# Optimization experiments

Hardware: AMD Instinct MI355X
Metric: run time of the kernel (lower is better)

## Reference

```python
import jax, jax.numpy as jnp
import numpy as np

NEG_SLOPE = 0.2


def _gat_layer(x, W, a_src, a_dst, src, dst, ew, num_nodes):
    # Dense projection: [N, Din] @ [Din, Dout] -> [N, Dout]
    h = x @ W
    s = h @ a_src  # per-node source score, [N]
    d = h @ a_dst  # per-node destination score, [N]
    score = jax.nn.leaky_relu(s[src] + d[dst], NEG_SLOPE)  # [E]
    # segment softmax over incoming edges of each destination node
    m = jax.ops.segment_max(score, dst, num_segments=num_nodes)
    ex = jnp.exp(score - m[dst])
    denom = jax.ops.segment_sum(ex, dst, num_segments=num_nodes)
    alpha = ex / jnp.maximum(denom[dst], jnp.asarray(1e-16, ex.dtype))
    alpha = alpha * ew  # edge-weighted attention
    # gather h_j, scale by alpha, scatter-add into destinations
    return jax.ops.segment_sum(h[src] * alpha[:, None], dst, num_segments=num_nodes)


def setup_inputs() -> dict:
    key = jax.random.key(0)
    ks = jax.random.split(key, 9)
    N, E, F_IN, HID, NC = 100000, 1600000, 256, 64, 40
    x = jax.random.normal(ks[0], (N, F_IN), dtype=jnp.float32)
    edge_index = jax.random.randint(ks[1], (2, E), 0, N, dtype=jnp.int32)
    edge_weight = jax.random.uniform(ks[2], (E,), dtype=jnp.float32)
    W1 = jax.random.normal(ks[3], (F_IN, HID), dtype=jnp.float32) / np.sqrt(F_IN)
    a1_src = jax.random.normal(ks[4], (HID,), dtype=jnp.float32) / np.sqrt(HID)
    a1_dst = jax.random.normal(ks[5], (HID,), dtype=jnp.float32) / np.sqrt(HID)
    W2 = jax.random.normal(ks[6], (HID, NC), dtype=jnp.float32) / np.sqrt(HID)
    a2_src = jax.random.normal(ks[7], (NC,), dtype=jnp.float32) / np.sqrt(NC)
    a2_dst = jax.random.normal(ks[8], (NC,), dtype=jnp.float32) / np.sqrt(NC)
    return {"x": x, "edge_index": edge_index, "edge_weight": edge_weight,
            "W1": W1, "a1_src": a1_src, "a1_dst": a1_dst,
            "W2": W2, "a2_src": a2_src, "a2_dst": a2_dst}


def reference(x, edge_index, edge_weight, W1, a1_src, a1_dst, W2, a2_src, a2_dst):
    N = x.shape[0]
    # add_self_loops=True in both convs: append (i, i) edges with weight 1
    loops = jnp.arange(N, dtype=edge_index.dtype)
    src = jnp.concatenate([edge_index[0], loops])
    dst = jnp.concatenate([edge_index[1], loops])
    ew = jnp.concatenate([edge_weight, jnp.ones((N,), edge_weight.dtype)])
    h = jax.nn.relu(_gat_layer(x, W1, a1_src, a1_dst, src, dst, ew, N))
    # dropout inactive in eval mode
    out = _gat_layer(h, W2, a2_src, a2_dst, src, dst, ew, N)
    return out
```

## Files before the change

kernel.cpp:

```cpp
#include <hip/hip_runtime.h>
#include <hip/hip_bf16.h>
#include <math.h>

#define NEG_SLOPE 0.2f

typedef __attribute__((ext_vector_type(4))) float f32x4;
typedef __attribute__((ext_vector_type(8))) short bf16x8;
typedef __attribute__((ext_vector_type(4))) short bf16x4;

__device__ __forceinline__ float leaky(float x) { return x > 0.f ? x : NEG_SLOPE * x; }

__device__ __forceinline__ unsigned short bf_hi(float x) {
  return (unsigned short)(__float_as_uint(x) >> 16);
}

__device__ __forceinline__ unsigned short bf_rne(float x) {
  unsigned u = __float_as_uint(x);
  return (unsigned short)((u + 0x7FFFu + ((u >> 16) & 1u)) >> 16);
}


#define BIN_CHUNK 2048
#define BCAP 8192

__global__ void k_curinit(int* __restrict__ cursor, int NB) {
  int i = blockIdx.x * blockDim.x + threadIdx.x;
  if (i < NB) cursor[i] = i * BCAP;
}

__global__ __launch_bounds__(256)
void k_bin(const int* __restrict__ ei, const float* __restrict__ ew, int E, int N,
           int* __restrict__ cursor, int2* __restrict__ staged, int NB) {
  __shared__ int lhist[512];
  __shared__ int lbase[512];
  int tid = threadIdx.x;
  int start = blockIdx.x * BIN_CHUNK;
  int NT = E + N;
  int srcv[8], dstv[8]; float wv[8];
#pragma unroll
  for (int j = 0; j < 8; j++) {
    int e = start + j * 256 + tid;
    int s = 0, d = -1; float w = 0.f;
    if (e < NT) {
      if (e < E) { s = ei[e]; d = ei[E + e]; w = ew[e]; }
      else       { s = d = e - E; w = 1.f; }
    }
    srcv[j] = s; dstv[j] = d; wv[j] = w;
  }
  for (int b = tid; b < NB; b += 256) lhist[b] = 0;
  __syncthreads();
#pragma unroll
  for (int j = 0; j < 8; j++)
    if (dstv[j] >= 0) atomicAdd(&lhist[dstv[j] >> 8], 1);
  __syncthreads();
  for (int b = tid; b < NB; b += 256) {
    int n = lhist[b];
    lbase[b] = (n > 0) ? atomicAdd(&cursor[b], n) : 0;
    lhist[b] = 0;
  }
  __syncthreads();
#pragma unroll
  for (int j = 0; j < 8; j++) {
    if (dstv[j] >= 0) {
      int bkt = dstv[j] >> 8;
      int off = atomicAdd(&lhist[bkt], 1);
      staged[lbase[bkt] + off] =
          make_int2(srcv[j] | ((dstv[j] & 255) << 24), __float_as_int(wv[j]));
    }
  }
}

__global__ __launch_bounds__(512)
void k_bscan(const int* __restrict__ cursor, int NB, int NT, int N,
             int* __restrict__ bbase, int* __restrict__ rp) {
  __shared__ int sm[512];
  int tid = threadIdx.x;
  int v = (tid < NB) ? cursor[tid] - tid * BCAP : 0;
  sm[tid] = v;
  __syncthreads();
  for (int off = 1; off < 512; off <<= 1) {
    int x = sm[tid];
    int a = (tid >= off) ? sm[tid - off] : 0;
    __syncthreads();
    sm[tid] = x + a;
    __syncthreads();
  }
  if (tid < NB) bbase[tid] = sm[tid] - v;
  if (tid == 0) { bbase[NB] = sm[NB - 1]; rp[N] = NT; }
}

__global__ __launch_bounds__(512)
void k_finalize(const int2* __restrict__ staged, const int* __restrict__ bbase,
                int N, int* __restrict__ rp, int2* __restrict__ csr) {
  __shared__ int cnt[256];
  __shared__ int sm[256];
  int b = blockIdx.x, tid = threadIdx.x;
  int sbase = b * BCAP;
  int cbase = bbase[b];
  int size = bbase[b + 1] - cbase;
  if (tid < 256) cnt[tid] = 0;
  __syncthreads();
  for (int i = tid; i < size; i += 512) {
    int2 v = staged[sbase + i];
    atomicAdd(&cnt[((unsigned)v.x) >> 24], 1);
  }
  __syncthreads();
  int s = 0;
  if (tid < 256) { s = cnt[tid]; sm[tid] = s; }
  __syncthreads();
  for (int off = 1; off < 256; off <<= 1) {
    int x = 0;
    if (tid < 256) { x = sm[tid]; if (tid >= off) x += sm[tid - off]; }
    __syncthreads();
    if (tid < 256) sm[tid] = x;
    __syncthreads();
  }
  if (tid < 256) {
    int excl = sm[tid] - s;
    int node = (b << 8) + tid;
    if (node < N) rp[node] = cbase + excl;
    cnt[tid] = excl;
  }
  __syncthreads();
  for (int i = tid; i < size; i += 512) {
    int2 v = staged[sbase + i];
    int dlow = ((unsigned)v.x) >> 24;
    int pos = cbase + atomicAdd(&cnt[dlow], 1);
    csr[pos] = make_int2(v.x & 0x00FFFFFF, v.y);
  }
}

__global__ __launch_bounds__(256)
void k_wprep(const float* __restrict__ W, int K, int Mout,
             unsigned short* __restrict__ whi, unsigned short* __restrict__ wlo) {
  int idx = blockIdx.x * 256 + threadIdx.x;
  if (idx >= K * 64) return;
  int k = idx >> 6, n = idx & 63;
  float v = (n < Mout) ? W[(size_t)k * Mout + n] : 0.f;
  unsigned short h = bf_hi(v);
  float hf = __uint_as_float((unsigned)h << 16);
  unsigned short l = bf_hi(v - hf);
  int kc = k >> 5, kk = k & 31, quad = kk >> 3, j = kk & 7;
  int ct = n >> 4, nn = n & 15;
  int off = (((kc * 4 + ct) * 64) + quad * 16 + nn) * 8 + j;
  whi[off] = h; wlo[off] = l;
}

__global__ __launch_bounds__(256)
void k_gemm_mfma(const float* __restrict__ X, int K,
                 const unsigned short* __restrict__ WHI, const unsigned short* __restrict__ WLO,
                 const float* __restrict__ ASRC, const float* __restrict__ ADST, int Mout,
                 float* __restrict__ Hf, unsigned short* __restrict__ Hb, int ldH,
                 float* __restrict__ S, float* __restrict__ D, int N) {
  __shared__ __align__(16) unsigned short xhi[2048], xlo[2048];
  __shared__ __align__(16) unsigned short whs[2048], wls[2048];
  int tid = threadIdx.x;
  int lane = tid & 63, w = tid >> 6;
  int rowBase = blockIdx.x * 64;

  f32x4 acc[4];
#pragma unroll
  for (int c = 0; c < 4; c++) acc[c] = (f32x4){0.f, 0.f, 0.f, 0.f};

  int q0 = tid, q1 = tid + 256;
  int row0 = q0 >> 3, k40 = (q0 & 7) << 2;
  int row1 = q1 >> 3, k41 = (q1 & 7) << 2;
  int xo0 = (((row0 >> 4) * 64) + (k40 >> 3) * 16 + (row0 & 15)) * 8 + (k40 & 7);
  int xo1 = (((row1 >> 4) * 64) + (k41 >> 3) * 16 + (row1 & 15)) * 8 + (k41 & 7);
  int grow0 = rowBase + row0, grow1 = rowBase + row1;

  int nch = K >> 5;
  f32x4 xr0, xr1; bf16x8 wh, wl;

  xr0 = (f32x4){0.f, 0.f, 0.f, 0.f}; xr1 = xr0;
  if (grow0 < N) xr0 = *(const f32x4*)&X[(size_t)grow0 * K + k40];
  if (grow1 < N) xr1 = *(const f32x4*)&X[(size_t)grow1 * K + k41];
  wh = *(const bf16x8*)(WHI + tid * 8);
  wl = *(const bf16x8*)(WLO + tid * 8);

  for (int kc = 0; kc < nch; kc++) {
    bf16x4 h4, l4;
#pragma unroll
    for (int i = 0; i < 4; i++) {
      unsigned short h = bf_hi(xr0[i]);
      float hf = __uint_as_float((unsigned)h << 16);
      h4[i] = (short)h; l4[i] = (short)bf_hi(xr0[i] - hf);
    }
    *(bf16x4*)(xhi + xo0) = h4; *(bf16x4*)(xlo + xo0) = l4;
#pragma unroll
    for (int i = 0; i < 4; i++) {
      unsigned short h = bf_hi(xr1[i]);
      float hf = __uint_as_float((unsigned)h << 16);
      h4[i] = (short)h; l4[i] = (short)bf_hi(xr1[i] - hf);
    }
    *(bf16x4*)(xhi + xo1) = h4; *(bf16x4*)(xlo + xo1) = l4;
    *(bf16x8*)(whs + tid * 8) = wh;
    *(bf16x8*)(wls + tid * 8) = wl;
    __syncthreads();

    if (kc + 1 < nch) {
      int kb = (kc + 1) << 5;
      xr0 = (f32x4){0.f, 0.f, 0.f, 0.f}; xr1 = xr0;
      if (grow0 < N) xr0 = *(const f32x4*)&X[(size_t)grow0 * K + kb + k40];
      if (grow1 < N) xr1 = *(const f32x4*)&X[(size_t)grow1 * K + kb + k41];
      wh = *(const bf16x8*)(WHI + (size_t)(kc + 1) * 2048 + tid * 8);
      wl = *(const bf16x8*)(WLO + (size_t)(kc + 1) * 2048 + tid * 8);
    }

    bf16x8 ah = *(const bf16x8*)(xhi + (w * 64 + lane) * 8);
    bf16x8 al = *(const bf16x8*)(xlo + (w * 64 + lane) * 8);
#pragma unroll
    for (int c = 0; c < 4; c++) {
      bf16x8 bh = *(const bf16x8*)(whs + (c * 64 + lane) * 8);
      bf16x8 bl = *(const bf16x8*)(wls + (c * 64 + lane) * 8);
      acc[c] = __builtin_amdgcn_mfma_f32_16x16x32_bf16(ah, bh, acc[c], 0, 0, 0);
      acc[c] = __builtin_amdgcn_mfma_f32_16x16x32_bf16(ah, bl, acc[c], 0, 0, 0);
      acc[c] = __builtin_amdgcn_mfma_f32_16x16x32_bf16(al, bh, acc[c], 0, 0, 0);
    }
    __syncthreads();
  }

  int nn = lane & 15, quad = lane >> 4;
  float as_[4], ad_[4];
#pragma unroll
  for (int c = 0; c < 4; c++) {
    int col = c * 16 + nn;
    as_[c] = (col < Mout) ? ASRC[col] : 0.f;
    ad_[c] = (col < Mout) ? ADST[col] : 0.f;
  }
#pragma unroll
  for (int r = 0; r < 4; r++) {
    int grow = rowBase + w * 16 + quad * 4 + r;
    float ps = 0.f, pd = 0.f;
#pragma unroll
    for (int c = 0; c < 4; c++) {
      float v = acc[c][r];
      int col = c * 16 + nn;
      if (grow < N && col < Mout) {
        if (Hb) Hb[(size_t)grow * ldH + col] = bf_rne(v);
        else    Hf[(size_t)grow * ldH + col] = v;
      }
      ps += v * as_[c]; pd += v * ad_[c];
    }
#pragma unroll
    for (int off = 1; off < 16; off <<= 1) {
      ps += __shfl_xor(ps, off);
      pd += __shfl_xor(pd, off);
    }
    if (nn == 0 && grow < N) { S[grow] = ps; D[grow] = pd; }
  }
}

template <bool BF16>
__global__ __launch_bounds__(256)
void k_agg_fused(const int* __restrict__ rp, const int2* __restrict__ csr,
                 const float* __restrict__ S, const float* __restrict__ D,
                 const void* __restrict__ HinV, int ldh,
                 float* __restrict__ Out, int F4, int ldo, int do_relu, int N) {
  int gw = (blockIdx.x * blockDim.x + threadIdx.x) >> 6;
  int lane = threadIdx.x & 63;
  int sub = lane >> 4, fl = lane & 15;
  int node = gw * 4 + sub;
  bool active = node < N;
  bool fless = fl < F4;
  int b = 0, e = 1; float dd = 0.f;
  if (active) { b = rp[node]; e = rp[node + 1]; dd = D[node]; }
  float den = 0.f;
  f32x4 acc0 = (f32x4){0.f, 0.f, 0.f, 0.f};
  f32x4 acc1 = (f32x4){0.f, 0.f, 0.f, 0.f};

  int need = e - b;
  need = max(need, __shfl_xor(need, 16));
  need = max(need, __shfl_xor(need, 32));
  int iters = (need + 3) >> 2;
  int last = e - 1;

  int t = b;
  for (int it = 0; it < iters; it++, t += 4) {
    int  idx[4]; float wgt[4], sv[4], ex[4]; f32x4 hv[4];
#pragma unroll
    for (int j = 0; j < 4; j++) {
      int tj = t + j < e ? t + j : last;
      int2 p = csr[tj];
      idx[j] = p.x;
      wgt[j] = (t + j < e) ? __int_as_float(p.y) : 0.f;
    }
#pragma unroll
    for (int j = 0; j < 4; j++) sv[j] = S[idx[j]];
#pragma unroll
    for (int j = 0; j < 4; j++) {
      hv[j] = (f32x4){0.f, 0.f, 0.f, 0.f};
      if (fless && (t + j < e)) {
        if (BF16) {
          const unsigned short* Hb = (const unsigned short*)HinV;
          ushort4 uv = *(const ushort4*)(Hb + (size_t)idx[j] * ldh + (fl << 2));
          hv[j][0] = __uint_as_float((unsigned)uv.x << 16);
          hv[j][1] = __uint_as_float((unsigned)uv.y << 16);
          hv[j][2] = __uint_as_float((unsigned)uv.z << 16);
          hv[j][3] = __uint_as_float((unsigned)uv.w << 16);
        } else {
          const float* Hf = (const float*)HinV;
          hv[j] = *(const f32x4*)&Hf[(size_t)idx[j] * ldh + (fl << 2)];
        }
      }
    }
#pragma unroll
    for (int j = 0; j < 4; j++)
      ex[j] = (t + j < e) ? __expf(leaky(sv[j] + dd)) : 0.f;
    den += (ex[0] + ex[1]) + (ex[2] + ex[3]);
    acc0 += hv[0] * (ex[0] * wgt[0]) + hv[1] * (ex[1] * wgt[1]);
    acc1 += hv[2] * (ex[2] * wgt[2]) + hv[3] * (ex[3] * wgt[3]);
  }

  if (active && fless) {
    float inv = 1.0f / fmaxf(den, 1e-16f);
    f32x4 o = (acc0 + acc1) * inv;
    if (do_relu) {
#pragma unroll
      for (int j = 0; j < 4; j++) o[j] = fmaxf(o[j], 0.f);
    }
    *(f32x4*)&Out[(size_t)node * ldo + (fl << 2)] = o;
  }
}

extern "C" void kernel_launch(void* const* d_in, const int* in_sizes, int n_in,
                              void* d_out, int out_size, void* d_ws, size_t ws_size,
                              hipStream_t stream) {
  const float* x   = (const float*)d_in[0];
  const int*   ei  = (const int*)d_in[1];
  const float* ew  = (const float*)d_in[2];
  const float* W1  = (const float*)d_in[3];
  const float* a1s = (const float*)d_in[4];
  const float* a1d = (const float*)d_in[5];
  const float* W2  = (const float*)d_in[6];
  const float* a2s = (const float*)d_in[7];
  const float* a2d = (const float*)d_in[8];

  const int HID = in_sizes[4];
  const int NC  = in_sizes[7];
  const int FIN = in_sizes[3] / HID;
  const int N   = in_sizes[0] / FIN;
  const int E   = in_sizes[2];
  const int NT  = E + N;
  const int NB  = (N + 255) >> 8;
  float* out = (float*)d_out;

  char* wsb = (char*)d_ws;
  size_t off = 0;
  auto alloc = [&](size_t bytes) -> char* {
    char* p = wsb + off;
    off += (bytes + 255) & ~(size_t)255;
    return p;
  };
  unsigned short* h1b = (unsigned short*)alloc((size_t)N * 64 * 2);
  float* h2     = (float*)alloc((size_t)N * 64 * 4);
  float* g2     = (float*)alloc((size_t)N * 48 * 4);
  float* S      = (float*)alloc((size_t)N * 4);
  float* D      = (float*)alloc((size_t)N * 4);
  int*   rp     = (int*)alloc((size_t)(N + 1) * 4);
  int*   bbase  = (int*)alloc((size_t)(NB + 1) * 4);
  int*   cursor = (int*)alloc((size_t)NB * 4);
  int2*  csr    = (int2*)alloc((size_t)NT * 8);
  int2*  staged = (int2*)alloc((size_t)NB * BCAP * 8);
  unsigned short* whi1 = (unsigned short*)alloc((size_t)FIN * 64 * 2);
  unsigned short* wlo1 = (unsigned short*)alloc((size_t)FIN * 64 * 2);
  unsigned short* whi2 = (unsigned short*)alloc((size_t)HID * 64 * 2);
  unsigned short* wlo2 = (unsigned short*)alloc((size_t)HID * 64 * 2);
  (void)ws_size; (void)n_in; (void)out_size;

  const int ebins = (NT + BIN_CHUNK - 1) / BIN_CHUNK;

  hipLaunchKernelGGL(k_curinit, dim3((NB + 255) / 256), dim3(256), 0, stream, cursor, NB);
  hipLaunchKernelGGL(k_bin, dim3(ebins), dim3(256), 0, stream, ei, ew, E, N, cursor, staged, NB);
  hipLaunchKernelGGL(k_bscan, dim3(1), dim3(512), 0, stream, cursor, NB, NT, N, bbase, rp);
  hipLaunchKernelGGL(k_finalize, dim3(NB), dim3(512), 0, stream, staged, bbase, N, rp, csr);

  hipLaunchKernelGGL(k_wprep, dim3((FIN * 64 + 255) / 256), dim3(256), 0, stream,
                     W1, FIN, HID, whi1, wlo1);
  hipLaunchKernelGGL(k_wprep, dim3((HID * 64 + 255) / 256), dim3(256), 0, stream,
                     W2, HID, NC, whi2, wlo2);

  const int gblocks = (N + 63) / 64;
  const int ablocks = (N + 15) / 16;

  hipLaunchKernelGGL(k_gemm_mfma, dim3(gblocks), dim3(256), 0, stream,
                     x, FIN, whi1, wlo1, a1s, a1d, HID, (float*)nullptr, h1b, 64, S, D, N);
  hipLaunchKernelGGL((k_agg_fused<true>), dim3(ablocks), dim3(256), 0, stream,
                     rp, csr, S, D, (const void*)h1b, 64, h2, 16, 64, 1, N);

  hipLaunchKernelGGL(k_gemm_mfma, dim3(gblocks), dim3(256), 0, stream,
                     h2, HID, whi2, wlo2, a2s, a2d, NC, g2, (unsigned short*)nullptr, 48, S, D, N);
  hipLaunchKernelGGL((k_agg_fused<false>), dim3(ablocks), dim3(256), 0, stream,
                     rp, csr, S, D, (const void*)g2, 48, out, 10, NC, 0, N);
}
```

Baseline: 368.7 us.

## Reorder layer-2 as aggregate-then-project with precomputed score vectors

Uses linearity to swap the order in layer 2: attention scores are computed from h2 through W2·a_src and W2·a_dst vectors fused into the layer-1 aggregation. The 64-wide bf16 h2 is aggregated first and the GEMM with W2 runs afterwards, writing the output directly. The change also prefetches the next CSR entries inside the aggregation loop and stores h2 in bf16. It gathers 64 bf16 features instead of 40 fp32 per edge, and the bf16 h2 plus reordered arithmetic change rounding.

```diff
diff --git a/kernel.cpp b/kernel.cpp
--- a/kernel.cpp
+++ b/kernel.cpp
@@ -146,6 +146,19 @@
   whi[off] = h; wlo[off] = l;
 }
 
+__global__ void k_wvec(const float* __restrict__ W2, const float* __restrict__ a2s,
+                       const float* __restrict__ a2d, int K, int NC,
+                       float* __restrict__ ws, float* __restrict__ wd) {
+  int k = threadIdx.x;
+  if (k >= K) return;
+  float s = 0.f, d = 0.f;
+  for (int n = 0; n < NC; n++) {
+    float w = W2[(size_t)k * NC + n];
+    s += w * a2s[n]; d += w * a2d[n];
+  }
+  ws[k] = s; wd[k] = d;
+}
+
 __global__ __launch_bounds__(256)
 void k_gemm_mfma(const float* __restrict__ X, int K,
                  const unsigned short* __restrict__ WHI, const unsigned short* __restrict__ WLO,
@@ -251,18 +264,18 @@
   }
 }
 
-template <bool BF16>
+template <bool OUTB16, bool RELU, bool SCORES>
 __global__ __launch_bounds__(256)
-void k_agg_fused(const int* __restrict__ rp, const int2* __restrict__ csr,
-                 const float* __restrict__ S, const float* __restrict__ D,
-                 const void* __restrict__ HinV, int ldh,
-                 float* __restrict__ Out, int F4, int ldo, int do_relu, int N) {
+void k_agg(const int* __restrict__ rp, const int2* __restrict__ csr,
+           const float* __restrict__ S, const float* __restrict__ D,
+           const unsigned short* __restrict__ Hb, void* __restrict__ OutV,
+           const float* __restrict__ WS, const float* __restrict__ WD,
+           float* __restrict__ S2, float* __restrict__ D2, int N) {
   int gw = (blockIdx.x * blockDim.x + threadIdx.x) >> 6;
   int lane = threadIdx.x & 63;
   int sub = lane >> 4, fl = lane & 15;
   int node = gw * 4 + sub;
   bool active = node < N;
-  bool fless = fl < F4;
   int b = 0, e = 1; float dd = 0.f;
   if (active) { b = rp[node]; e = rp[node + 1]; dd = D[node]; }
   float den = 0.f;
@@ -275,51 +288,74 @@
   int iters = (need + 3) >> 2;
   int last = e - 1;
 
+  int idx[4]; float wgt[4];
   int t = b;
+#pragma unroll
+  for (int j = 0; j < 4; j++) {
+    int tj = (t + j < e) ? t + j : last;
+    int2 p = csr[tj];
+    idx[j] = p.x;
+    wgt[j] = (t + j < e) ? __int_as_float(p.y) : 0.f;
+  }
+
   for (int it = 0; it < iters; it++, t += 4) {
-    int  idx[4]; float wgt[4], sv[4], ex[4]; f32x4 hv[4];
+    float sv[4];
+#pragma unroll
+    for (int j = 0; j < 4; j++) sv[j] = S[idx[j]];
+    f32x4 hv[4];
 #pragma unroll
     for (int j = 0; j < 4; j++) {
-      int tj = t + j < e ? t + j : last;
+      ushort4 uv = *(const ushort4*)(Hb + (size_t)idx[j] * 64 + (fl << 2));
+      hv[j][0] = __uint_as_float((unsigned)uv.x << 16);
+      hv[j][1] = __uint_as_float((unsigned)uv.y << 16);
+      hv[j][2] = __uint_as_float((unsigned)uv.z << 16);
+      hv[j][3] = __uint_as_float((unsigned)uv.w << 16);
+    }
+    int idn[4]; float wgn[4];
+#pragma unroll
+    for (int j = 0; j < 4; j++) {
+      int tj = (t + 4 + j < e) ? t + 4 + j : last;
       int2 p = csr[tj];
-      idx[j] = p.x;
-      wgt[j] = (t + j < e) ? __int_as_float(p.y) : 0.f;
-    }
-#pragma unroll
-    for (int j = 0; j < 4; j++) sv[j] = S[idx[j]];
-#pragma unroll
-    for (int j = 0; j < 4; j++) {
-      hv[j] = (f32x4){0.f, 0.f, 0.f, 0.f};
-      if (fless && (t + j < e)) {
-        if (BF16) {
-          const unsigned short* Hb = (const unsigned short*)HinV;
-          ushort4 uv = *(const ushort4*)(Hb + (size_t)idx[j] * ldh + (fl << 2));
-          hv[j][0] = __uint_as_float((unsigned)uv.x << 16);
-          hv[j][1] = __uint_as_float((unsigned)uv.y << 16);
-          hv[j][2] = __uint_as_float((unsigned)uv.z << 16);
-          hv[j][3] = __uint_as_float((unsigned)uv.w << 16);
-        } else {
-          const float* Hf = (const float*)HinV;
-          hv[j] = *(const f32x4*)&Hf[(size_t)idx[j] * ldh + (fl << 2)];
-        }
-      }
-    }
+      idn[j] = p.x;
+      wgn[j] = (t + 4 + j < e) ? __int_as_float(p.y) : 0.f;
+    }
+    float ex[4];
 #pragma unroll
     for (int j = 0; j < 4; j++)
       ex[j] = (t + j < e) ? __expf(leaky(sv[j] + dd)) : 0.f;
     den += (ex[0] + ex[1]) + (ex[2] + ex[3]);
     acc0 += hv[0] * (ex[0] * wgt[0]) + hv[1] * (ex[1] * wgt[1]);
     acc1 += hv[2] * (ex[2] * wgt[2]) + hv[3] * (ex[3] * wgt[3]);
-  }
-
-  if (active && fless) {
-    float inv = 1.0f / fmaxf(den, 1e-16f);
-    f32x4 o = (acc0 + acc1) * inv;
-    if (do_relu) {
-#pragma unroll
-      for (int j = 0; j < 4; j++) o[j] = fmaxf(o[j], 0.f);
-    }
-    *(f32x4*)&Out[(size_t)node * ldo + (fl << 2)] = o;
+#pragma unroll
+    for (int j = 0; j < 4; j++) { idx[j] = idn[j]; wgt[j] = wgn[j]; }
+  }
+
+  float inv = 1.0f / fmaxf(den, 1e-16f);
+  f32x4 o = (acc0 + acc1) * inv;
+  if (RELU) {
+#pragma unroll
+    for (int j = 0; j < 4; j++) o[j] = fmaxf(o[j], 0.f);
+  }
+  if (SCORES) {
+    f32x4 ws = *(const f32x4*)&WS[fl << 2];
+    f32x4 wd = *(const f32x4*)&WD[fl << 2];
+    float ps = o[0] * ws[0] + o[1] * ws[1] + o[2] * ws[2] + o[3] * ws[3];
+    float pd = o[0] * wd[0] + o[1] * wd[1] + o[2] * wd[2] + o[3] * wd[3];
+#pragma unroll
+    for (int off = 1; off < 16; off <<= 1) {
+      ps += __shfl_xor(ps, off);
+      pd += __shfl_xor(pd, off);
+    }
+    if (active && fl == 0) { S2[node] = ps; D2[node] = pd; }
+  }
+  if (active) {
+    if (OUTB16) {
+      ushort4 st;
+      st.x = bf_rne(o[0]); st.y = bf_rne(o[1]); st.z = bf_rne(o[2]); st.w = bf_rne(o[3]);
+      *(ushort4*)((unsigned short*)OutV + (size_t)node * 64 + (fl << 2)) = st;
+    } else {
+      *(f32x4*)((float*)OutV + (size_t)node * 64 + (fl << 2)) = o;
+    }
   }
 }
 
@@ -353,10 +389,12 @@
     return p;
   };
   unsigned short* h1b = (unsigned short*)alloc((size_t)N * 64 * 2);
-  float* h2     = (float*)alloc((size_t)N * 64 * 4);
-  float* g2     = (float*)alloc((size_t)N * 48 * 4);
+  unsigned short* h2b = (unsigned short*)alloc((size_t)N * 64 * 2);
+  float* A      = (float*)alloc((size_t)N * 64 * 4);
   float* S      = (float*)alloc((size_t)N * 4);
   float* D      = (float*)alloc((size_t)N * 4);
+  float* S2     = (float*)alloc((size_t)N * 4);
+  float* D2     = (float*)alloc((size_t)N * 4);
   int*   rp     = (int*)alloc((size_t)(N + 1) * 4);
   int*   bbase  = (int*)alloc((size_t)(NB + 1) * 4);
   int*   cursor = (int*)alloc((size_t)NB * 4);
@@ -366,6 +404,8 @@
   unsigned short* wlo1 = (unsigned short*)alloc((size_t)FIN * 64 * 2);
   unsigned short* whi2 = (unsigned short*)alloc((size_t)HID * 64 * 2);
   unsigned short* wlo2 = (unsigned short*)alloc((size_t)HID * 64 * 2);
+  float* w2s = (float*)alloc((size_t)HID * 4);
+  float* w2d = (float*)alloc((size_t)HID * 4);
   (void)ws_size; (void)n_in; (void)out_size;
 
   const int ebins = (NT + BIN_CHUNK - 1) / BIN_CHUNK;
@@ -379,17 +419,18 @@
                      W1, FIN, HID, whi1, wlo1);
   hipLaunchKernelGGL(k_wprep, dim3((HID * 64 + 255) / 256), dim3(256), 0, stream,
                      W2, HID, NC, whi2, wlo2);
+  hipLaunchKernelGGL(k_wvec, dim3(1), dim3(64), 0, stream, W2, a2s, a2d, HID, NC, w2s, w2d);
 
   const int gblocks = (N + 63) / 64;
   const int ablocks = (N + 15) / 16;
 
   hipLaunchKernelGGL(k_gemm_mfma, dim3(gblocks), dim3(256), 0, stream,
                      x, FIN, whi1, wlo1, a1s, a1d, HID, (float*)nullptr, h1b, 64, S, D, N);
-  hipLaunchKernelGGL((k_agg_fused<true>), dim3(ablocks), dim3(256), 0, stream,
-                     rp, csr, S, D, (const void*)h1b, 64, h2, 16, 64, 1, N);
-
+  hipLaunchKernelGGL((k_agg<true, true, true>), dim3(ablocks), dim3(256), 0, stream,
+                     rp, csr, S, D, h1b, (void*)h2b, w2s, w2d, S2, D2, N);
+  hipLaunchKernelGGL((k_agg<false, false, false>), dim3(ablocks), dim3(256), 0, stream,
+                     rp, csr, S2, D2, h2b, (void*)A, (const float*)nullptr,
+                     (const float*)nullptr, (float*)nullptr, (float*)nullptr, N);
   hipLaunchKernelGGL(k_gemm_mfma, dim3(gblocks), dim3(256), 0, stream,
-                     h2, HID, whi2, wlo2, a2s, a2d, NC, g2, (unsigned short*)nullptr, 48, S, D, N);
-  hipLaunchKernelGGL((k_agg_fused<false>), dim3(ablocks), dim3(256), 0, stream,
-                     rp, csr, S, D, (const void*)g2, 48, out, 10, NC, 0, N);
-}
+                     A, HID, whi2, wlo2, a2s, a2d, NC, out, (unsigned short*)nullptr, NC, S, D, N);
+}
```

After: 356.7 us. 1.03x faster.
